# Kernel tuning notes

Measured on AMD Instinct MI355X. Metric: run time of the kernel, lower is better.

## Reference

```python
import jax, jax.numpy as jnp
import numpy as np
from jax import lax

DN = ('NCHW', 'OIHW', 'NCHW')


def _conv(x, w, b, stride, pad):
    y = lax.conv_general_dilated(x, w, (stride, stride), [(pad, pad), (pad, pad)],
                                 dimension_numbers=DN)
    return y + b[None, :, None, None]


def _deconv(x, w, b, stride, pad):
    # torch ConvTranspose2d weight: (in, out, kH, kW). Equivalent forward conv:
    # flip spatially, swap in/out, dilate input by stride, pad by k-1-pad.
    k = w.shape[2]
    kern = jnp.flip(w, (2, 3)).transpose(1, 0, 2, 3)  # (out, in, kH, kW)
    p = k - 1 - pad
    y = lax.conv_general_dilated(x, kern, (1, 1), [(p, p), (p, p)],
                                 lhs_dilation=(stride, stride), dimension_numbers=DN)
    return y + b[None, :, None, None]


def setup_inputs() -> dict:
    key = jax.random.key(0)
    ks = jax.random.split(key, 16)
    s = 0.05
    D, K, H = 64, 512, 128  # embedding_dim, num_embeddings, hidden_channels
    inp = {
        'x': jax.random.uniform(ks[0], (16, 3, 256, 256), dtype=jnp.float32),
        'conv1_w': jax.random.normal(ks[1], (H, 3, 4, 4), jnp.float32) * s,
        'conv1_b': jnp.zeros((H,), jnp.float32),
        'conv2_w': jax.random.normal(ks[2], (H, H, 4, 4), jnp.float32) * s,
        'conv2_b': jnp.zeros((H,), jnp.float32),
        'conv3_w': jax.random.normal(ks[3], (D, H, 3, 3), jnp.float32) * s,
        'conv3_b': jnp.zeros((D,), jnp.float32),
        'emb': jax.random.normal(ks[4], (K, D), jnp.float32),
        'deconv1_w': jax.random.normal(ks[5], (D, H, 4, 4), jnp.float32) * s,
        'deconv1_b': jnp.zeros((H,), jnp.float32),
        'deconv2_w': jax.random.normal(ks[6], (H, H, 4, 4), jnp.float32) * s,
        'deconv2_b': jnp.zeros((H,), jnp.float32),
        'deconv3_w': jax.random.normal(ks[7], (H, 3, 3, 3), jnp.float32) * s,
        'deconv3_b': jnp.zeros((3,), jnp.float32),
    }
    return inp


def reference(x, conv1_w, conv1_b, conv2_w, conv2_b, conv3_w, conv3_b, emb,
              deconv1_w, deconv1_b, deconv2_w, deconv2_b, deconv3_w, deconv3_b):
    # Encoder
    h = jax.nn.relu(_conv(x, conv1_w, conv1_b, 2, 1))
    h = jax.nn.relu(_conv(h, conv2_w, conv2_b, 2, 1))
    z_e = _conv(h, conv3_w, conv3_b, 1, 1)  # (B, 64, 64, 64)

    # Vector quantizer (faithful to torch: flatten NCHW directly to (-1, D))
    D = emb.shape[1]
    flat = z_e.reshape(-1, D)  # (N, D)
    d = (jnp.sum(flat * flat, axis=1, keepdims=True)
         + jnp.sum(emb * emb, axis=1)
         - 2.0 * flat @ emb.T)  # (N, K)
    indices = jnp.argmin(d, axis=1)[:, None]  # (N, 1)
    z_q = emb[indices[:, 0]].reshape(z_e.shape)

    # Decoder
    g = jax.nn.relu(_deconv(z_q, deconv1_w, deconv1_b, 2, 1))
    g = jax.nn.relu(_deconv(g, deconv2_w, deconv2_b, 2, 1))
    x_recon = jax.nn.sigmoid(_deconv(g, deconv3_w, deconv3_b, 1, 1))
    return (x_recon, indices, z_q)
```

## Files before the change

kernel.cpp:

```cpp
#include <hip/hip_runtime.h>
#include <hip/hip_bf16.h>

#define DEV __device__ __forceinline__

typedef __attribute__((ext_vector_type(8))) short bf16x8;
typedef __attribute__((ext_vector_type(4))) float f32x4;
typedef __attribute__((ext_vector_type(4))) unsigned short u16x4;

#define MFMA16(a,b,c) __builtin_amdgcn_mfma_f32_16x16x32_bf16(a,b,c,0,0,0)

DEV unsigned short bfbits(float v){ __hip_bfloat16 h = __float2bfloat16(v); return *(unsigned short*)&h; }
DEV float bf2f(unsigned short u){ __hip_bfloat16 h = *(__hip_bfloat16*)&u; return __bfloat162float(h); }
DEV void split3(float v, unsigned short& h, unsigned short& m, unsigned short& l) {
  h = bfbits(v);        float r  = v - bf2f(h);
  m = bfbits(r);        float r2 = r - bf2f(m);
  l = bfbits(r2);
}
DEV uint4 zero4(){ uint4 z; z.x=0; z.y=0; z.z=0; z.w=0; return z; }
DEV void gload_lds16(const void* g, void* l) {
  __builtin_amdgcn_global_load_lds(
      (const __attribute__((address_space(1))) void*)g,
      (__attribute__((address_space(3))) void*)l, 16, 0, 0);
}

DEV void prep_deconv_img(int i, int CI, const float* __restrict__ w, unsigned short* __restrict__ w2) {
  const int nch = CI/16;
  int cil = i & 7, s = (i >> 3) & 7, co = (i >> 6) & 127, f = (i >> 13) & 1;
  int rest = i >> 14;
  int ch = rest % nch, e = rest / nch;
  int k = ch*64 + s*8 + cil;
  int ci = (k & 15) | ((k >> 6) << 4);
  int tap = (k >> 4) & 3, a = tap >> 1, b = tap & 1;
  float v = w[ (((long)ci*128 + co)*4 + (2*a+1-e))*4 + (2*b+1-f) ];
  w2[(long)(e*nch + ch)*16384 + ((long)(f*128 + co))*64 + ((s ^ (co&7))*8) + cil] = bfbits(v);
}
__global__ __launch_bounds__(256) void wprep_all(
    const float* __restrict__ c1w, float* __restrict__ w2c1,
    const float* __restrict__ c2w, unsigned short* __restrict__ w2c2,
    const float* __restrict__ c3w, unsigned short* __restrict__ w2c3,
    const float* __restrict__ d1w, unsigned short* __restrict__ w2d1,
    const float* __restrict__ d2w, unsigned short* __restrict__ w2d2,
    const float* __restrict__ d3w, unsigned short* __restrict__ w2d3,
    const float* __restrict__ emb, float* __restrict__ esq) {
  const int bx = blockIdx.x, t = threadIdx.x;
  if (bx < 24) {
    int i = bx*256 + t;
    if (i < 6144) {
      int tap = i & 15, ci = (i>>4) % 3, co = i / 48;
      w2c1[((long)ci*16 + tap)*128 + co] = c1w[i];
    }
  } else if (bx < 1048) {
    int i = (bx-24)*256 + t;
    int cil = i & 7, s = (i>>3) & 15, co = (i>>7) & 63;
    int ch = (i>>13) & 15, cog = i >> 17;
    int co_g = cog*64 + co, ci = ch*8 + cil, ky = s >> 2, kx = s & 3;
    float v = c2w[(((long)co_g*128 + ci)*4 + ky)*4 + kx];
    unsigned short h,m,l; split3(v,h,m,l);
    long base = (long)(cog*16 + ch)*24576 + ((long)co*16 + (s ^ (co&15)))*8 + cil;
    w2c2[base] = h; w2c2[base + 8192] = m; w2c2[base + 16384] = l;
  } else if (bx < 1432) {
    int i = (bx-1048)*256 + t;
    int k = i % 1536, co = i / 1536;
    int ch = k / 96, rem = k % 96;
    int tap = rem >> 3, cil = rem & 7;
    int ci = ch*8 + cil, ky = tap >> 2, kx = tap & 3;
    float v = (kx < 3) ? c3w[(((long)co*128 + ci)*3 + ky)*3 + kx] : 0.f;
    unsigned short h,m,l; split3(v,h,m,l);
    long base = (long)ch*24576 + ((long)co*16 + (tap ^ (co&15)))*8 + cil;
    w2c3[base] = h; w2c3[base + 8192] = m; w2c3[base + 16384] = l;
  } else if (bx < 1944) {
    prep_deconv_img((bx-1432)*256 + t, 64, d1w, w2d1);
  } else if (bx < 2968) {
    prep_deconv_img((bx-1944)*256 + t, 128, d2w, w2d2);
  } else if (bx < 3064) {
    int i = (bx-2968)*256 + t;
    if (i < 24576) {
      int k = i % 1536, co = i / 1536;
      int ch = k / 96, rem = k % 96;
      int tap = rem >> 3, cil = rem & 7;
      int ci = ch*8 + cil, ky = tap >> 2, kx = tap & 3;
      float v = (co < 3 && kx < 3) ? d3w[(((long)ci*3 + co)*3 + ky)*3 + kx] : 0.f;
      w2d3[i] = bfbits(v);
    }
  } else {
    int code = (bx-3064)*256 + t;
    if (code < 512) {
      const float4* ev = (const float4*)(emb + (long)code*64);
      float s = 0.f;
      #pragma unroll
      for (int q=0;q<16;q++){ float4 e4 = ev[q];
        s += e4.x*e4.x + e4.y*e4.y + e4.z*e4.z + e4.w*e4.w; }
      esq[code] = s;
    }
  }
}

__global__ __launch_bounds__(256) void conv1_split(
    const float* __restrict__ x, const float* __restrict__ w2,
    const float* __restrict__ bias, unsigned short* __restrict__ h1, long PS1) {
  __shared__ __align__(16) float sIn[3][18][20];
  __shared__ __align__(16) float sW[3*16*64];
  const int tid = threadIdx.x;
  const int b = blockIdx.z >> 1, cog = blockIdx.z & 1;
  const int co0 = cog*64;
  const int oy0 = blockIdx.y*8, ox0 = blockIdx.x*8;
  const int cg2 = tid >> 5;
  const int pg2 = tid & 31;
  const int r = pg2 >> 2, pxp = (pg2 & 3)*2;
  float acc[8][2];
  #pragma unroll
  for (int c=0;c<8;c++){ float bv = bias[co0 + cg2*8 + c];
    acc[c][0]=bv; acc[c][1]=bv; }
  const float* xb = x + (long)b*3*256*256;
  const int iy0 = 2*oy0 - 1, ix0 = 2*ox0 - 1;
  for (int t=tid; t<3*18*18; t+=256) {
    int xx = t%18, yy=(t/18)%18, ci=t/324;
    int gy = iy0+yy, gx = ix0+xx;
    float v = 0.f;
    if (gy>=0 && gy<256 && gx>=0 && gx<256) v = xb[((long)ci*256+gy)*256+gx];
    sIn[ci][yy][xx] = v;
  }
  for (int t=tid; t<3*16*64; t+=256) {
    sW[t] = w2[(long)(t>>6)*128 + co0 + (t&63)];
  }
  __syncthreads();
  for (int ci=0; ci<3; ci++) {
    #pragma unroll
    for (int ky=0;ky<4;ky++)
    #pragma unroll
    for (int kx=0;kx<4;kx++) {
      const float* wp = &sW[(ci*16 + ky*4+kx)*64 + cg2*8];
      float4 w0 = *(const float4*)wp;
      float4 w1 = *(const float4*)(wp+4);
      const int yy = 2*r + ky;
      #pragma unroll
      for (int p=0;p<2;p++) {
        float iv = sIn[ci][yy][2*(pxp+p)+kx];
        acc[0][p] += w0.x*iv; acc[1][p] += w0.y*iv;
        acc[2][p] += w0.z*iv; acc[3][p] += w0.w*iv;
        acc[4][p] += w1.x*iv; acc[5][p] += w1.y*iv;
        acc[6][p] += w1.z*iv; acc[7][p] += w1.w*iv;
      }
    }
  }
  const int chg = cog*8 + cg2;
  #pragma unroll
  for (int p=0;p<2;p++) {
    unsigned short th[8], tm[8], tl[8];
    #pragma unroll
    for (int c=0;c<8;c++) {
      float v = fmaxf(acc[c][p], 0.f);
      split3(v, th[c], tm[c], tl[c]);
    }
    long base = (((long)(b*128 + oy0+r)*16 + chg)*128 + ox0+pxp+p)*8;
    *(uint4*)(h1 + base)          = *(uint4*)th;
    *(uint4*)(h1 + PS1 + base)    = *(uint4*)tm;
    *(uint4*)(h1 + 2*PS1 + base)  = *(uint4*)tl;
  }
}

__global__ __launch_bounds__(256, 2) void conv2_mfma(
    const unsigned short* __restrict__ h1, long PS1,
    const unsigned short* __restrict__ w2,
    const float* __restrict__ bias,
    unsigned short* __restrict__ h2, long PS2) {
  __shared__ __align__(16) unsigned short sA[3][4][130][8];
  __shared__ __align__(16) unsigned short sB[24576];
  const int tid = threadIdx.x;
  const int oy = blockIdx.x, cog = blockIdx.y, b = blockIdx.z;
  const int wave = tid >> 6, lane = tid & 63;
  const int wr = wave >> 1, wc = wave & 1;
  const int col_l = lane & 15, kg = lane >> 4;
  const int iy0 = 2*oy - 1;
  f32x4 acc[2][2] = {};
  unsigned short* sAf = &sA[0][0][0][0];
  const unsigned short* bsrc = w2 + (long)cog*16*24576;

  int aOff[6], aLdsO[6]; bool aOk[6];
  #pragma unroll
  for (int j = 0; j < 6; ++j) {
    int idx = tid + j*256;
    int px = idx & 127, rr = (idx >> 7) & 3, pl = idx >> 9;
    int iy = iy0 + rr;
    aOk[j] = (iy >= 0 && iy < 128);
    aOff[j] = (int)(pl*PS1 + (long)(b*128 + (aOk[j]?iy:0))*16384 + px*8);
    aLdsO[j] = ((pl*4 + rr)*130 + px + 1)*8;
  }
  uint4 pA[6];
  #pragma unroll
  for (int j=0;j<6;j++)  pA[j] = aOk[j] ? *(const uint4*)(h1 + aOff[j]) : zero4();

  if (tid < 24) {
    int pl = tid>>3, rr=(tid>>1)&3, c=tid&1;
    *(uint4*)&sA[pl][rr][c?129:0][0] = zero4();
  }

  for (int ch = 0; ch < 16; ++ch) {
    __syncthreads();
    #pragma unroll
    for (int j=0;j<6;j++)  *(uint4*)(sAf + aLdsO[j]) = pA[j];
    #pragma unroll
    for (int j = 0; j < 12; ++j) {
      int blk = wave*12 + j;
      gload_lds16(bsrc + (long)ch*24576 + blk*512 + lane*8, &sB[blk*512]);
    }
    if (ch < 15) {
      #pragma unroll
      for (int j=0;j<6;j++)  pA[j] = aOk[j] ? *(const uint4*)(h1 + aOff[j] + (ch+1)*1024) : zero4();
    }
    __syncthreads();
    #pragma unroll
    for (int s = 0; s < 4; ++s) {
      bf16x8 aF[2][3]; bf16x8 bF[2][3];
      const int tap = s*4 + kg;
      #pragma unroll
      for (int mf = 0; mf < 2; ++mf) {
        int ox = wr*32 + mf*16 + col_l;
        #pragma unroll
        for (int pl = 0; pl < 3; ++pl)
          aF[mf][pl] = *(const bf16x8*)&sA[pl][s][2*ox + kg][0];
      }
      #pragma unroll
      for (int nf = 0; nf < 2; ++nf) {
        int co = wc*32 + nf*16 + col_l;
        int ba = (co*16 + (tap ^ (co&15)))*8;
        bF[nf][0] = *(const bf16x8*)&sB[ba];
        bF[nf][1] = *(const bf16x8*)&sB[ba + 8192];
        bF[nf][2] = *(const bf16x8*)&sB[ba + 16384];
      }
      __builtin_amdgcn_s_setprio(1);
      #pragma unroll
      for (int mf = 0; mf < 2; ++mf)
      #pragma unroll
      for (int nf = 0; nf < 2; ++nf) {
        f32x4 a = acc[mf][nf];
        a = MFMA16(aF[mf][0], bF[nf][0], a);
        a = MFMA16(aF[mf][0], bF[nf][1], a);
        a = MFMA16(aF[mf][1], bF[nf][0], a);
        a = MFMA16(aF[mf][0], bF[nf][2], a);
        a = MFMA16(aF[mf][2], bF[nf][0], a);
        a = MFMA16(aF[mf][1], bF[nf][1], a);
        acc[mf][nf] = a;
      }
      __builtin_amdgcn_s_setprio(0);
    }
  }
  __syncthreads();
  #pragma unroll
  for (int nf = 0; nf < 2; ++nf) {
    int co = wc*32 + nf*16 + col_l;
    float bv = bias[cog*64 + co];
    #pragma unroll
    for (int mf = 0; mf < 2; ++mf) {
      int px0 = wr*32 + mf*16 + kg*4;
      u16x4 oh, om, ol;
      #pragma unroll
      for (int r = 0; r < 4; ++r) {
        float v = fmaxf(acc[mf][nf][r] + bv, 0.f);
        unsigned short h,m,l; split3(v,h,m,l);
        oh[r]=h; om[r]=m; ol[r]=l;
      }
      *(u16x4*)&sB[(0*64 + co)*72 + px0] = oh;
      *(u16x4*)&sB[(1*64 + co)*72 + px0] = om;
      *(u16x4*)&sB[(2*64 + co)*72 + px0] = ol;
    }
  }
  __syncthreads();
  #pragma unroll
  for (int j = 0; j < 6; ++j) {
    int idx = tid + j*256;
    int pl = idx >> 9, co_l = (idx >> 3) & 63, q = idx & 7;
    uint4 v = *(const uint4*)&sB[(pl*64 + co_l)*72 + q*8];
    *(uint4*)(h2 + (long)pl*PS2 + ((long)(b*128 + cog*64 + co_l)*64 + oy)*64 + q*8) = v;
  }
}

__global__ __launch_bounds__(256, 2) void conv3_mfma(
    const unsigned short* __restrict__ h2, long PS2,
    const unsigned short* __restrict__ w2,
    const float* __restrict__ bias,
    unsigned short* __restrict__ zeH, unsigned short* __restrict__ zeM,
    unsigned short* __restrict__ zeL) {
  __shared__ __align__(16) unsigned short sA[3*67*24];
  __shared__ __align__(16) unsigned short sB[24576];
  const int tid = threadIdx.x;
  const int oy = blockIdx.x, b = blockIdx.z;
  const int wave = tid >> 6, lane = tid & 63;
  const int wr = wave >> 1, wc = wave & 1;
  const int col_l = lane & 15, kg = lane >> 4;
  f32x4 acc[2][2] = {};
  for (int i = tid; i < 3*3*24; i += 256) {
    int j = i % 24, c = (i/24) % 3, rr = i/72;
    int col = (c==0) ? 0 : (c==1 ? 65 : 66);
    sA[(rr*67 + col)*24 + j] = 0;
  }
  const int li = tid & 7, rrA = (tid>>3)%3, ciA = tid/24;
  const int iyA = oy + rrA - 1;
  const bool aAct = (tid < 192);
  const bool aOk = aAct && (iyA >= 0 && iyA < 64);
  const long aBase = ((long)(b*128 + ciA)*64 + (aOk?iyA:0))*64 + li*8;
  uint4 ph, pm, pl4;
  ph = aOk ? *(const uint4*)(h2 + aBase) : zero4();
  pm = aOk ? *(const uint4*)(h2 + PS2 + aBase) : zero4();
  pl4 = aOk ? *(const uint4*)(h2 + 2*PS2 + aBase) : zero4();

  for (int ch = 0; ch < 16; ++ch) {
    __syncthreads();
    if (aAct) {
      const unsigned short* vh = (const unsigned short*)&ph;
      const unsigned short* vm = (const unsigned short*)&pm;
      const unsigned short* vl = (const unsigned short*)&pl4;
      #pragma unroll
      for (int p = 0; p < 8; ++p) {
        int pp = (p + li) & 7;
        int col = li*8 + pp + 1;
        int base = (rrA*67 + col)*24 + ciA;
        sA[base]      = vh[pp];
        sA[base + 8]  = vm[pp];
        sA[base + 16] = vl[pp];
      }
    }
    #pragma unroll
    for (int j = 0; j < 12; ++j) {
      int blk = wave*12 + j;
      gload_lds16(w2 + (long)ch*24576 + blk*512 + lane*8, &sB[blk*512]);
    }
    if (ch < 15) {
      long nb = aBase + (long)(ch+1)*32768;
      ph = aOk ? *(const uint4*)(h2 + nb) : zero4();
      pm = aOk ? *(const uint4*)(h2 + PS2 + nb) : zero4();
      pl4 = aOk ? *(const uint4*)(h2 + 2*PS2 + nb) : zero4();
    }
    __syncthreads();
    #pragma unroll
    for (int s = 0; s < 3; ++s) {
      bf16x8 aF[2][3]; bf16x8 bF[2][3];
      const int tap = s*4 + kg;
      #pragma unroll
      for (int mf = 0; mf < 2; ++mf) {
        int ox = wr*32 + mf*16 + col_l;
        int base = (s*67 + ox + kg)*24;
        aF[mf][0] = *(const bf16x8*)&sA[base];
        aF[mf][1] = *(const bf16x8*)&sA[base+8];
        aF[mf][2] = *(const bf16x8*)&sA[base+16];
      }
      #pragma unroll
      for (int nf = 0; nf < 2; ++nf) {
        int co = wc*32 + nf*16 + col_l;
        int ba = (co*16 + (tap ^ (co&15)))*8;
        bF[nf][0] = *(const bf16x8*)&sB[ba];
        bF[nf][1] = *(const bf16x8*)&sB[ba + 8192];
        bF[nf][2] = *(const bf16x8*)&sB[ba + 16384];
      }
      __builtin_amdgcn_s_setprio(1);
      #pragma unroll
      for (int mf = 0; mf < 2; ++mf)
      #pragma unroll
      for (int nf = 0; nf < 2; ++nf) {
        f32x4 a = acc[mf][nf];
        a = MFMA16(aF[mf][0], bF[nf][0], a);
        a = MFMA16(aF[mf][0], bF[nf][1], a);
        a = MFMA16(aF[mf][1], bF[nf][0], a);
        a = MFMA16(aF[mf][0], bF[nf][2], a);
        a = MFMA16(aF[mf][2], bF[nf][0], a);
        a = MFMA16(aF[mf][1], bF[nf][1], a);
        acc[mf][nf] = a;
      }
      __builtin_amdgcn_s_setprio(0);
    }
  }
  __syncthreads();
  #pragma unroll
  for (int nf = 0; nf < 2; ++nf) {
    int co = wc*32 + nf*16 + col_l;
    float bv = bias[co];
    #pragma unroll
    for (int mf = 0; mf < 2; ++mf) {
      int px0 = wr*32 + mf*16 + kg*4;
      u16x4 oh, om, ol;
      #pragma unroll
      for (int r = 0; r < 4; ++r) {
        float v = acc[mf][nf][r] + bv;
        unsigned short h,m,l; split3(v,h,m,l);
        oh[r]=h; om[r]=m; ol[r]=l;
      }
      *(u16x4*)&sB[(0*64 + co)*72 + px0] = oh;
      *(u16x4*)&sB[(1*64 + co)*72 + px0] = om;
      *(u16x4*)&sB[(2*64 + co)*72 + px0] = ol;
    }
  }
  __syncthreads();
  #pragma unroll
  for (int j = 0; j < 6; ++j) {
    int idx = tid + j*256;
    int pl = idx >> 9, co_l = (idx >> 3) & 63, q = idx & 7;
    uint4 v = *(const uint4*)&sB[(pl*64 + co_l)*72 + q*8];
    unsigned short* dst = (pl==0) ? zeH : ((pl==1) ? zeM : zeL);
    *(uint4*)(dst + ((long)(b*64 + co_l)*64 + oy)*64 + q*8) = v;
  }
}

template<int TX, int MODE>
struct SmemD {
  union {
    struct { __align__(16) unsigned short In[2][TX+2][24];
             __align__(16) unsigned short W[2*128*64]; } o;
    struct { __align__(16) unsigned short In[2][TX+2][16];
             __align__(16) unsigned short W[2*128*64]; } v;
    __align__(16) unsigned short Out[2*TX][136];
  };
};

template<int CIN, int TX, int MODE>
__global__ __launch_bounds__(TX*4, (TX==64)?3:4) void deconv_mfma(
    const void* __restrict__ xin, const unsigned short* __restrict__ w2,
    const float* __restrict__ bias, unsigned short* __restrict__ yI) {
  constexpr int NTHR = TX*4;
  constexpr int NWAVE = NTHR/64;
  constexpr int NWG  = 32/NWAVE;
  __shared__ SmemD<TX,MODE> sm;
  unsigned short* Wb = MODE ? &sm.v.W[0] : &sm.o.W[0];

  const int tid = threadIdx.x;
  const int ty = blockIdx.x, e = blockIdx.y, b = blockIdx.z;
  const int wave = tid >> 6, lane = tid & 63;
  const int wc = wave & 1, wr = wave >> 1;
  const int f = (wr*64) / TX;
  const int tx_base = (wr*64) & (TX-1);
  const int col_l = lane & 15, kg = lane >> 4;
  const unsigned short* wsrc = w2 + (long)e*(CIN/16)*16384;

  constexpr int TPR = NTHR/32;
  const int rowid = tid / TPR, liO = tid % TPR;
  const int sci = rowid >> 1, srr = rowid & 1;
  float4 pLo, pHi; uint4 pIn;
  long aBase = 0; bool aOk = false;
  int pxV = 0, halfV = 0, rrV = 0;
  if (MODE == 0) {
    int iy = ty + e - 1 + srr;
    aOk = (iy >= 0 && iy < TX);
    aBase = ((long)b*CIN + sci)*TX*TX + (long)(aOk?iy:0)*TX + liO*8;
    if (aOk) { const float4* s4 = (const float4*)((const float*)xin + aBase);
               pLo = s4[0]; pHi = s4[1]; }
  } else {
    halfV = tid & 1; pxV = (tid >> 1) & (TX-1); rrV = tid >> 8;
    int iy = ty + e - 1 + rrV;
    aOk = (iy >= 0 && iy < TX);
    aBase = ((long)b*TX + (aOk?iy:0))*((long)(CIN/8)*TX*8) + (long)halfV*TX*8 + pxV*8;
    pIn = aOk ? *(const uint4*)((const unsigned short*)xin + aBase) : zero4();
  }

  if (MODE == 0) {
    if (tid < 64) {
      int rr = tid & 1, cc = ((tid>>1)&1) ? TX+1 : 0, ci = tid >> 2;
      sm.o.In[rr][cc][ci] = 0;
    }
  } else {
    if (tid < 8) {
      int rr = tid & 1, c = (tid>>1)&1, hf = (tid>>2)&1;
      *(uint4*)&sm.v.In[rr][c?TX+1:0][hf*8] = zero4();
    }
  }

  f32x4 acc[4][4] = {};
  for (int ch = 0; ch < CIN/16; ++ch) {
    __syncthreads();
    if (MODE == 0) {
      unsigned short vals[8];
      if (aOk) {
        float4 lo = pLo, hi = pHi;
        vals[0]=bfbits(lo.x); vals[1]=bfbits(lo.y); vals[2]=bfbits(lo.z); vals[3]=bfbits(lo.w);
        vals[4]=bfbits(hi.x); vals[5]=bfbits(hi.y); vals[6]=bfbits(hi.z); vals[7]=bfbits(hi.w);
      } else {
        #pragma unroll
        for (int j=0;j<8;j++) vals[j] = 0;
      }
      #pragma unroll
      for (int j=0;j<8;j++) {
        int jj = (j + liO) & 7;
        sm.o.In[srr][1 + liO*8 + jj][sci] = vals[jj];
      }
    } else {
      *(uint4*)&sm.v.In[rrV][pxV+1][halfV*8] = pIn;
    }
    #pragma unroll
    for (int j = 0; j < NWG; ++j) {
      int blk = wave*NWG + j;
      gload_lds16(wsrc + (long)ch*16384 + blk*512 + lane*8, Wb + blk*512);
    }
    if (ch + 1 < CIN/16) {
      if (MODE == 0) {
        if (aOk) { const float4* s4 = (const float4*)((const float*)xin + aBase + (long)(ch+1)*16*TX*TX);
                   pLo = s4[0]; pHi = s4[1]; }
      } else {
        pIn = aOk ? *(const uint4*)((const unsigned short*)xin + aBase + (ch+1)*2*TX*8) : zero4();
      }
    }
    __syncthreads();
    #pragma unroll
    for (int kk = 0; kk < 2; ++kk) {
      bf16x8 aF[4];
      const int tap = kk*2 + (kg >> 1), a = tap >> 1, bb = tap & 1;
      #pragma unroll
      for (int mf = 0; mf < 4; ++mf) {
        int tx = tx_base + mf*16 + col_l;
        if (MODE == 0) aF[mf] = *(const bf16x8*)&sm.o.In[1-a][tx + 1 + f - bb][(kg&1)*8];
        else           aF[mf] = *(const bf16x8*)&sm.v.In[1-a][tx + 1 + f - bb][(kg&1)*8];
      }
      const int slot = kk*4 + kg;
      __builtin_amdgcn_s_setprio(1);
      #pragma unroll
      for (int nf = 0; nf < 4; ++nf) {
        int co_l = nf*16 + col_l;
        bf16x8 bF = *(const bf16x8*)(Wb + (f*128 + wc*64 + co_l)*64 + (slot ^ (co_l & 7))*8);
        #pragma unroll
        for (int mf = 0; mf < 4; ++mf)
          acc[mf][nf] = MFMA16(aF[mf], bF, acc[mf][nf]);
      }
      __builtin_amdgcn_s_setprio(0);
    }
  }

  __syncthreads();
  float bv[4];
  #pragma unroll
  for (int nf = 0; nf < 4; ++nf) bv[nf] = bias[wc*64 + nf*16 + col_l];
  #pragma unroll
  for (int mf = 0; mf < 4; ++mf)
  #pragma unroll
  for (int nf = 0; nf < 4; ++nf) {
    int co = wc*64 + nf*16 + col_l;
    #pragma unroll
    for (int r = 0; r < 4; ++r) {
      int tx = tx_base + mf*16 + kg*4 + r;
      float v = fmaxf(acc[mf][nf][r] + bv[nf], 0.f);
      int ox = 2*tx + f;
      sm.Out[ox][co ^ (((ox>>3)&7)<<3)] = bfbits(v);
    }
  }
  __syncthreads();
  const int oy = 2*ty + e;
  #pragma unroll
  for (int j = 0; j < 8; ++j) {
    int i = tid + j*NTHR;
    int px = i & (2*TX-1), chn = i / (2*TX);
    uint4 vv = *(const uint4*)&sm.Out[px][(chn*8) ^ (((px>>3)&7)<<3)];
    *(uint4*)(yI + ((((long)b*(2*TX) + oy)*16 + chn)*(2*TX) + px)*8) = vv;
  }
}

__global__ __launch_bounds__(256, 2) void deconv3_mfma(
    const unsigned short* __restrict__ g2I,
    const unsigned short* __restrict__ w2,
    const float* __restrict__ bias, float* __restrict__ y) {
  __shared__ __align__(16) unsigned short sA[3][260][8];
  __shared__ __align__(16) unsigned short sB[16*12*16*8];
  const int tid = threadIdx.x;
  const int oy = blockIdx.x, b = blockIdx.y;
  const int wave = tid >> 6, lane = tid & 63;
  const int col_l = lane & 15, kg = lane >> 4;
  const int pxb = wave*64;
  for (int i = tid; i < 3072; i += 256) {
    int co = i & 15, tap = (i>>4) % 12, ch = i/192;
    *(uint4*)&sB[((ch*12+tap)*16+co)*8] = *(const uint4*)(w2 + (long)co*1536 + ch*96 + tap*8);
  }
  if (tid < 12) {
    int dy = tid >> 2, c = tid & 3;
    *(uint4*)&sA[dy][(c<2)?c:(256+c)][0] = zero4();
  }
  long aBase[3]; int aLdsO[3]; bool aOk[3];
  #pragma unroll
  for (int u = 0; u < 3; ++u) {
    int idx = tid + u*256;
    int px = idx & 255, dy = idx >> 8;
    int iy = oy - 1 + dy;
    aOk[u] = (iy >= 0 && iy < 256);
    aBase[u] = ((long)(b*256 + (aOk[u]?iy:0)))*32768 + px*8;
    aLdsO[u] = (dy*260 + px + 2)*8;
  }
  uint4 pA[3];
  #pragma unroll
  for (int u=0;u<3;u++) pA[u] = aOk[u] ? *(const uint4*)(g2I + aBase[u]) : zero4();

  unsigned short* sAf = &sA[0][0][0];
  f32x4 acc[4] = {};
  for (int ch = 0; ch < 16; ++ch) {
    __syncthreads();
    #pragma unroll
    for (int u=0;u<3;u++) *(uint4*)(sAf + aLdsO[u]) = pA[u];
    if (ch < 15) {
      #pragma unroll
      for (int u=0;u<3;u++)
        pA[u] = aOk[u] ? *(const uint4*)(g2I + aBase[u] + (ch+1)*2048) : zero4();
    }
    __syncthreads();
    #pragma unroll
    for (int s = 0; s < 3; ++s) {
      bf16x8 bF = *(const bf16x8*)&sB[((ch*12 + s*4 + kg)*16 + col_l)*8];
      __builtin_amdgcn_s_setprio(1);
      #pragma unroll
      for (int mf = 0; mf < 4; ++mf) {
        int px = pxb + mf*16 + col_l;
        bf16x8 aF = *(const bf16x8*)&sA[2-s][px + 3 - kg][0];
        acc[mf] = MFMA16(aF, bF, acc[mf]);
      }
      __builtin_amdgcn_s_setprio(0);
    }
  }
  if (col_l < 3) {
    float bv = bias[col_l];
    #pragma unroll
    for (int mf = 0; mf < 4; ++mf) {
      int px = pxb + mf*16 + kg*4;
      float4 o;
      o.x = 1.f/(1.f + expf(-(acc[mf][0] + bv)));
      o.y = 1.f/(1.f + expf(-(acc[mf][1] + bv)));
      o.z = 1.f/(1.f + expf(-(acc[mf][2] + bv)));
      o.w = 1.f/(1.f + expf(-(acc[mf][3] + bv)));
      *(float4*)(y + ((long)(b*3 + col_l)*256 + oy)*256 + px) = o;
    }
  }
}

__global__ __launch_bounds__(256, 2) void vq_mfma(
    const unsigned short* __restrict__ zeH, const unsigned short* __restrict__ zeM,
    const unsigned short* __restrict__ zeL,
    const float* __restrict__ emb, const float* __restrict__ esq,
    float* __restrict__ out_idx, float* __restrict__ zq) {
  __shared__ __align__(16) unsigned short sA[64*3*8*8];
  __shared__ __align__(16) unsigned short sB[128*3*8*8];
  __shared__ float snb[128];
  __shared__ int sidx[64];
  const int tid = threadIdx.x;
  const long n0 = (long)blockIdx.x*64;
  const int wave = tid >> 6, lane = tid & 63;
  const int col = lane & 15, kg = lane >> 4;

  #pragma unroll
  for (int j = 0; j < 6; ++j) {
    int idx = tid + j*256;
    int pl = idx >> 9, rem = idx & 511;
    int n = rem >> 3, slot = rem & 7;
    const unsigned short* src = (pl==0 ? zeH : (pl==1 ? zeM : zeL)) + (n0+n)*64 + slot*8;
    *(uint4*)&sA[((n*3 + pl)*8 + (slot ^ (n&7)))*8] = *(const uint4*)src;
  }

  const int codeT = tid >> 1, halfT = tid & 1;
  float4 pB[8];
  #pragma unroll
  for (int q = 0; q < 8; ++q)
    pB[q] = *(const float4*)(emb + (long)codeT*64 + halfT*32 + q*4);
  float pSn = (tid < 128) ? esq[tid] : 0.f;

  float best[4] = {3.4e38f,3.4e38f,3.4e38f,3.4e38f};
  int bidx[4] = {0,0,0,0};

  for (int ch = 0; ch < 4; ++ch) {
    __syncthreads();
    #pragma unroll
    for (int s4 = 0; s4 < 4; ++s4) {
      int slot = halfT*4 + s4;
      float4 lo = pB[s4*2], hi = pB[s4*2+1];
      unsigned short th[8], tm[8], tl[8];
      split3(lo.x, th[0], tm[0], tl[0]); split3(lo.y, th[1], tm[1], tl[1]);
      split3(lo.z, th[2], tm[2], tl[2]); split3(lo.w, th[3], tm[3], tl[3]);
      split3(hi.x, th[4], tm[4], tl[4]); split3(hi.y, th[5], tm[5], tl[5]);
      split3(hi.z, th[6], tm[6], tl[6]); split3(hi.w, th[7], tm[7], tl[7]);
      int base = ((codeT*3)*8 + (slot ^ (codeT&7)))*8;
      *(uint4*)&sB[base]       = *(uint4*)th;
      *(uint4*)&sB[base + 64]  = *(uint4*)tm;
      *(uint4*)&sB[base + 128] = *(uint4*)tl;
    }
    if (tid < 128) snb[tid] = pSn;
    if (ch < 3) {
      #pragma unroll
      for (int q = 0; q < 8; ++q)
        pB[q] = *(const float4*)(emb + ((long)(ch+1)*128 + codeT)*64 + halfT*32 + q*4);
      if (tid < 128) pSn = esq[(ch+1)*128 + tid];
    }
    __syncthreads();

    f32x4 acc[8] = {};
    #pragma unroll
    for (int kk = 0; kk < 2; ++kk) {
      const int nloc = wave*16 + col;
      const int slot = kk*4 + kg;
      bf16x8 aF[3];
      #pragma unroll
      for (int pl = 0; pl < 3; ++pl)
        aF[pl] = *(const bf16x8*)&sA[((nloc*3 + pl)*8 + (slot ^ (nloc&7)))*8];
      __builtin_amdgcn_s_setprio(1);
      #pragma unroll
      for (int cf = 0; cf < 8; ++cf) {
        int cl = cf*16 + col;
        int bb = ((cl*3)*8 + (slot ^ (cl&7)))*8;
        bf16x8 b0 = *(const bf16x8*)&sB[bb];
        bf16x8 b1 = *(const bf16x8*)&sB[bb + 64];
        bf16x8 b2 = *(const bf16x8*)&sB[bb + 128];
        f32x4 a = acc[cf];
        a = MFMA16(aF[0], b0, a);
        a = MFMA16(aF[0], b1, a);
        a = MFMA16(aF[1], b0, a);
        a = MFMA16(aF[0], b2, a);
        a = MFMA16(aF[2], b0, a);
        a = MFMA16(aF[1], b1, a);
        acc[cf] = a;
      }
      __builtin_amdgcn_s_setprio(0);
    }
    #pragma unroll
    for (int cf = 0; cf < 8; ++cf) {
      float sv = snb[cf*16 + col];
      int code = ch*128 + cf*16 + col;
      #pragma unroll
      for (int j = 0; j < 4; ++j) {
        float s = sv - 2.f*acc[cf][j];
        if (s < best[j]) { best[j] = s; bidx[j] = code; }
      }
    }
  }

  #pragma unroll
  for (int j = 0; j < 4; ++j) {
    float b = best[j]; int ii = bidx[j];
    #pragma unroll
    for (int off = 1; off < 16; off <<= 1) {
      float ob = __shfl_xor(b, off);
      int oi = __shfl_xor(ii, off);
      if (ob < b || (ob == b && oi < ii)) { b = ob; ii = oi; }
    }
    if (col == 0) sidx[wave*16 + kg*4 + j] = ii;
  }
  __syncthreads();
  if (tid < 64) out_idx[n0 + tid] = (float)sidx[tid];
  #pragma unroll
  for (int j = 0; j < 4; ++j) {
    int t = tid + j*256;
    int row = t >> 4, q = t & 15;
    float4 v = *(const float4*)(emb + (long)sidx[row]*64 + q*4);
    *(float4*)(zq + (n0 + row)*64 + q*4) = v;
  }
}

extern "C" void kernel_launch(void* const* d_in, const int* in_sizes, int n_in,
                              void* d_out, int out_size, void* d_ws, size_t ws_size,
                              hipStream_t stream) {
  const float* x   = (const float*)d_in[0];
  const float* c1w = (const float*)d_in[1];  const float* c1b = (const float*)d_in[2];
  const float* c2w = (const float*)d_in[3];  const float* c2b = (const float*)d_in[4];
  const float* c3w = (const float*)d_in[5];  const float* c3b = (const float*)d_in[6];
  const float* emb = (const float*)d_in[7];
  const float* d1w = (const float*)d_in[8];  const float* d1b = (const float*)d_in[9];
  const float* d2w = (const float*)d_in[10]; const float* d2b = (const float*)d_in[11];
  const float* d3w = (const float*)d_in[12]; const float* d3b = (const float*)d_in[13];
  float* out = (float*)d_out;

  float* xrec = out;
  float* oidx = out + 3145728;
  float* zq   = out + 3211264;

  const long XB  = 196608;
  const long ZEB = 262144;
  const long PS1 = 8388608;
  const long PS2 = 4194304;

  const size_t NEEDED = 112273408ULL;
  if (ws_size < NEEDED) return;
  char* wsb = (char*)d_ws;
  unsigned short* h1grp = (unsigned short*)wsb;
  unsigned short* g2grp = (unsigned short*)wsb;
  unsigned short* h2grp = (unsigned short*)(wsb + 67108864);
  unsigned short* g1grp = (unsigned short*)(wsb + 67108864);
  unsigned short* zeH = (unsigned short*)(wsb + 92274688);
  unsigned short* zeM = (unsigned short*)(wsb + 100663296);
  unsigned short* zeL = (unsigned short*)out;
  char* W = wsb + 109051904;
  float* w2c1          = (float*)(W);
  unsigned short* w2c2 = (unsigned short*)(W + 24576);
  unsigned short* w2c3 = (unsigned short*)(W + 1597440);
  unsigned short* w2d1 = (unsigned short*)(W + 2383872);
  unsigned short* w2d2 = (unsigned short*)(W + 2646016);
  unsigned short* w2d3 = (unsigned short*)(W + 3170304);
  float* esq           = (float*)(W + 3219456);

  wprep_all<<<3066, 256, 0, stream>>>(c1w, w2c1, c2w, w2c2, c3w, w2c3,
                                      d1w, w2d1, d2w, w2d2, d3w, w2d3, emb, esq);

  for (int g = 0; g < 4; ++g) {
    conv1_split<<<dim3(16,16,8), 256, 0, stream>>>(
        x + (long)g*4*XB, w2c1, c1b, h1grp, PS1);
    conv2_mfma<<<dim3(64,2,4), 256, 0, stream>>>(
        h1grp, PS1, w2c2, c2b, h2grp + (long)(g&1)*4*524288, PS2);
    if (g & 1) {
      long zo = (long)(g>>1)*8*ZEB;
      conv3_mfma<<<dim3(64,1,8), 256, 0, stream>>>(
          h2grp, PS2, w2c3, c3b, zeH + zo, zeM + zo, zeL + zo);
    }
  }
  vq_mfma<<<1024, 256, 0, stream>>>(zeH, zeM, zeL, emb, esq, oidx, zq);

  for (int g = 0; g < 4; ++g) {
    deconv_mfma<64, 64, 0 ><<<dim3(64, 2, 4), 256, 0, stream>>>(
        (const void*)(zq + (long)g*4*ZEB), w2d1, d1b, g1grp);
    deconv_mfma<128,128,1 ><<<dim3(128,2,4), 512, 0, stream>>>(
        (const void*)g1grp, w2d2, d2b, g2grp);
    deconv3_mfma<<<dim3(256,4), 256, 0, stream>>>(
        g2grp, w2d3, d3b, xrec + (long)g*4*XB);
  }
}
```

Measured before the change: 828.8 us.

## Store conv2 output channel-interleaved so conv3 loads A tiles via direct-to-LDS copies

conv2 now writes h2 in a layout where each pixel holds 8 consecutive channels per split plane (hi/mid/lo), with the transpose done through LDS at store time. conv3 then fills its A tile with global_load_lds instead of register loads followed by scattered per-element LDS stores, and zeroes halo and boundary rows up front. The aim is to remove conv3's register staging and its scalar LDS transpose. In exchange the register prefetch overlap is lost, conv2's epilogue now does strided 16-bit LDS reads, and boundary rows must stay zero across chunks.

```diff
diff --git a/kernel.cpp b/kernel.cpp
--- a/kernel.cpp
+++ b/kernel.cpp
@@ -163,7 +163,7 @@
     const unsigned short* __restrict__ h1, long PS1,
     const unsigned short* __restrict__ w2,
     const float* __restrict__ bias,
-    unsigned short* __restrict__ h2, long PS2) {
+    unsigned short* __restrict__ h2I) {
   __shared__ __align__(16) unsigned short sA[3][4][130][8];
   __shared__ __align__(16) unsigned short sB[24576];
   const int tid = threadIdx.x;
@@ -269,19 +269,21 @@
   #pragma unroll
   for (int j = 0; j < 6; ++j) {
     int idx = tid + j*256;
-    int pl = idx >> 9, co_l = (idx >> 3) & 63, q = idx & 7;
-    uint4 v = *(const uint4*)&sB[(pl*64 + co_l)*72 + q*8];
-    *(uint4*)(h2 + (long)pl*PS2 + ((long)(b*128 + cog*64 + co_l)*64 + oy)*64 + q*8) = v;
+    int pl = idx >> 9, ch = (idx >> 6) & 7, px = idx & 63;
+    unsigned short tmp[8];
+    #pragma unroll
+    for (int c = 0; c < 8; ++c) tmp[c] = sB[(pl*64 + ch*8 + c)*72 + px];
+    *(uint4*)(h2I + ((((long)(b*64 + oy)*3 + pl)*16 + cog*8 + ch)*64 + px)*8) = *(uint4*)tmp;
   }
 }
 
 __global__ __launch_bounds__(256, 2) void conv3_mfma(
-    const unsigned short* __restrict__ h2, long PS2,
+    const unsigned short* __restrict__ h2I,
     const unsigned short* __restrict__ w2,
     const float* __restrict__ bias,
     unsigned short* __restrict__ zeH, unsigned short* __restrict__ zeM,
     unsigned short* __restrict__ zeL) {
-  __shared__ __align__(16) unsigned short sA[3*67*24];
+  __shared__ __align__(16) unsigned short sA3[3][3][68][8];
   __shared__ __align__(16) unsigned short sB[24576];
   const int tid = threadIdx.x;
   const int oy = blockIdx.x, b = blockIdx.z;
@@ -289,35 +291,31 @@
   const int wr = wave >> 1, wc = wave & 1;
   const int col_l = lane & 15, kg = lane >> 4;
   f32x4 acc[2][2] = {};
-  for (int i = tid; i < 3*3*24; i += 256) {
-    int j = i % 24, c = (i/24) % 3, rr = i/72;
-    int col = (c==0) ? 0 : (c==1 ? 65 : 66);
-    sA[(rr*67 + col)*24 + j] = 0;
-  }
-  const int li = tid & 7, rrA = (tid>>3)%3, ciA = tid/24;
-  const int iyA = oy + rrA - 1;
-  const bool aAct = (tid < 192);
-  const bool aOk = aAct && (iyA >= 0 && iyA < 64);
-  const long aBase = ((long)(b*128 + ciA)*64 + (aOk?iyA:0))*64 + li*8;
-  uint4 ph, pm, pl4;
-  ph = aOk ? *(const uint4*)(h2 + aBase) : zero4();
-  pm = aOk ? *(const uint4*)(h2 + PS2 + aBase) : zero4();
-  pl4 = aOk ? *(const uint4*)(h2 + 2*PS2 + aBase) : zero4();
+  if (tid < 27) {
+    int row = tid/3, c = tid%3;
+    int pl = row/3, rr = row%3;
+    *(uint4*)&sA3[pl][rr][(c==0)?0:(64+c)][0] = zero4();
+  }
+  if (oy == 0 && tid < 192) {
+    int pl = tid >> 6, px = tid & 63;
+    *(uint4*)&sA3[pl][0][px+1][0] = zero4();
+  }
+  if (oy == 63 && tid < 192) {
+    int pl = tid >> 6, px = tid & 63;
+    *(uint4*)&sA3[pl][2][px+1][0] = zero4();
+  }
 
   for (int ch = 0; ch < 16; ++ch) {
     __syncthreads();
-    if (aAct) {
-      const unsigned short* vh = (const unsigned short*)&ph;
-      const unsigned short* vm = (const unsigned short*)&pm;
-      const unsigned short* vl = (const unsigned short*)&pl4;
-      #pragma unroll
-      for (int p = 0; p < 8; ++p) {
-        int pp = (p + li) & 7;
-        int col = li*8 + pp + 1;
-        int base = (rrA*67 + col)*24 + ciA;
-        sA[base]      = vh[pp];
-        sA[base + 8]  = vm[pp];
-        sA[base + 16] = vl[pp];
+    #pragma unroll
+    for (int j = 0; j < 3; ++j) {
+      int row = wave*3 + j;
+      if (row < 9) {
+        int pl = row/3, rr = row%3;
+        int iy = oy + rr - 1;
+        if (iy >= 0 && iy < 64)
+          gload_lds16(h2I + ((((long)(b*64 + iy)*3 + pl)*16 + ch)*64)*8 + lane*8,
+                      &sA3[pl][rr][1][0]);
       }
     }
     #pragma unroll
@@ -325,12 +323,6 @@
       int blk = wave*12 + j;
       gload_lds16(w2 + (long)ch*24576 + blk*512 + lane*8, &sB[blk*512]);
     }
-    if (ch < 15) {
-      long nb = aBase + (long)(ch+1)*32768;
-      ph = aOk ? *(const uint4*)(h2 + nb) : zero4();
-      pm = aOk ? *(const uint4*)(h2 + PS2 + nb) : zero4();
-      pl4 = aOk ? *(const uint4*)(h2 + 2*PS2 + nb) : zero4();
-    }
     __syncthreads();
     #pragma unroll
     for (int s = 0; s < 3; ++s) {
@@ -339,10 +331,9 @@
       #pragma unroll
       for (int mf = 0; mf < 2; ++mf) {
         int ox = wr*32 + mf*16 + col_l;
-        int base = (s*67 + ox + kg)*24;
-        aF[mf][0] = *(const bf16x8*)&sA[base];
-        aF[mf][1] = *(const bf16x8*)&sA[base+8];
-        aF[mf][2] = *(const bf16x8*)&sA[base+16];
+        #pragma unroll
+        for (int pl = 0; pl < 3; ++pl)
+          aF[mf][pl] = *(const bf16x8*)&sA3[pl][s][ox + kg][0];
       }
       #pragma unroll
       for (int nf = 0; nf < 2; ++nf) {
@@ -762,14 +753,14 @@
   const long XB  = 196608;
   const long ZEB = 262144;
   const long PS1 = 8388608;
-  const long PS2 = 4194304;
+  const long H2B = 1572864;
 
   const size_t NEEDED = 112273408ULL;
   if (ws_size < NEEDED) return;
   char* wsb = (char*)d_ws;
   unsigned short* h1grp = (unsigned short*)wsb;
   unsigned short* g2grp = (unsigned short*)wsb;
-  unsigned short* h2grp = (unsigned short*)(wsb + 67108864);
+  unsigned short* h2I   = (unsigned short*)(wsb + 67108864);
   unsigned short* g1grp = (unsigned short*)(wsb + 67108864);
   unsigned short* zeH = (unsigned short*)(wsb + 92274688);
   unsigned short* zeM = (unsigned short*)(wsb + 100663296);
@@ -790,11 +781,11 @@
     conv1_split<<<dim3(16,16,8), 256, 0, stream>>>(
         x + (long)g*4*XB, w2c1, c1b, h1grp, PS1);
     conv2_mfma<<<dim3(64,2,4), 256, 0, stream>>>(
-        h1grp, PS1, w2c2, c2b, h2grp + (long)(g&1)*4*524288, PS2);
+        h1grp, PS1, w2c2, c2b, h2I + (long)(g&1)*4*H2B);
     if (g & 1) {
       long zo = (long)(g>>1)*8*ZEB;
       conv3_mfma<<<dim3(64,1,8), 256, 0, stream>>>(
-          h2grp, PS2, w2c3, c3b, zeH + zo, zeM + zo, zeL + zo);
+          h2I, w2c3, c3b, zeH + zo, zeM + zo, zeL + zo);
     }
   }
   vq_mfma<<<1024, 256, 0, stream>>>(zeH, zeM, zeL, emb, esq, oidx, zq);
```

After: 746.2 us. 1.11x faster.
